# Optimization experiments

Measured on AMD Instinct MI355X. Metric: run time of the kernel, lower is better.

## Reference

```python
import jax, jax.numpy as jnp
import numpy as np

EMB = 512
HEADS = 8

def setup_inputs() -> dict:
    key = jax.random.key(0)
    ks = jax.random.split(key, 9)
    s = 1.0 / np.sqrt(EMB)
    x = jax.random.normal(ks[0], (32, 4096, EMB), dtype=jnp.float32)
    Wq = jax.random.normal(ks[1], (EMB, EMB), dtype=jnp.float32) * s
    bq = jax.random.normal(ks[2], (EMB,), dtype=jnp.float32) * s
    Wk = jax.random.normal(ks[3], (EMB, EMB), dtype=jnp.float32) * s
    bk = jax.random.normal(ks[4], (EMB,), dtype=jnp.float32) * s
    Wv = jax.random.normal(ks[5], (EMB, EMB), dtype=jnp.float32) * s
    bv = jax.random.normal(ks[6], (EMB,), dtype=jnp.float32) * s
    Wo = jax.random.normal(ks[7], (EMB, EMB), dtype=jnp.float32) * s
    bo = jax.random.normal(ks[8], (EMB,), dtype=jnp.float32) * s
    return {"x": x, "Wq": Wq, "bq": bq, "Wk": Wk, "bk": bk,
            "Wv": Wv, "bv": bv, "Wo": Wo, "bo": bo}

def reference(x, Wq, bq, Wk, bk, Wv, bv, Wo, bo):
    b, n, e = x.shape
    h = HEADS
    d = e // h
    scale = jnp.asarray(d ** 0.5, x.dtype)
    # torch Linear: y = x @ W.T + b
    q = (x @ Wq.T + bq).reshape(b, n, h, d)
    k = (x @ Wk.T + bk).reshape(b, n, h, d)
    v = (x @ Wv.T + bv).reshape(b, n, h, d)
    # NOTE: contracts over sequence axis n (faithful to original einsum),
    # producing a (b, h, d, d) feature-feature score matrix.
    qk = jnp.einsum('bnhq,bnhk->bhqk', q, k) / scale
    attn = jax.nn.softmax(qk, axis=-1)  # softmax over head_dim axis
    # dropout is identity at inference
    weighted = jnp.einsum('bhqk,bnhk->bnhq', attn, v).reshape(b, n, e)
    return weighted @ Wo.T + bo
```

## Files before the change

### kernel.cpp

```cpp
#include <hip/hip_runtime.h>
#include <hip/hip_bf16.h>
#include <stdint.h>

#define BATCH 32
#define SEQ   4096
#define EMB   512
#define HEADS 8
#define HD    64
#define SCALE 0.125f

typedef __attribute__((ext_vector_type(8))) short bf16x8;
typedef __attribute__((ext_vector_type(4))) float f32x4;

__device__ __forceinline__ unsigned short f2bf(float f) {
    union { float f; unsigned int u; } v; v.f = f;
    unsigned int u = v.u;
    return (unsigned short)((u + 0x7FFFu + ((u >> 16) & 1u)) >> 16);
}
__device__ __forceinline__ float bf2f(unsigned short h) {
    union { unsigned int u; float f; } v; v.u = ((unsigned int)h) << 16;
    return v.f;
}
__device__ __forceinline__ unsigned int cvtpk(float lo, float hi) {
    unsigned int r;
    asm("v_cvt_pk_bf16_f32 %0, %1, %2" : "=v"(r) : "v"(lo), "v"(hi));
    return r;
}
__device__ __forceinline__ float lo_as_f(unsigned int p) {
    union { unsigned int u; float f; } v; v.u = p << 16; return v.f;
}
__device__ __forceinline__ float hi_as_f(unsigned int p) {
    union { unsigned int u; float f; } v; v.u = p & 0xFFFF0000u; return v.f;
}

#define MFMA16(a, b, c) __builtin_amdgcn_mfma_f32_16x16x32_bf16((a), (b), (c), 0, 0, 0)

union F4 { float4 v; float f[4]; };
struct Regs { F4 a0, a1, a2, a3; };

template <int NCHUNK, bool XBF>
__global__ __launch_bounds__(1024) void k1_gram(const float* __restrict__ x,
                                                float* __restrict__ P,
                                                float* __restrict__ svp,
                                                unsigned short* __restrict__ xbf) {
  constexpr int KC  = SEQ / NCHUNK;
  constexpr int NIT = KC / 32;
  constexpr int NWG = BATCH * 4 * NCHUNK;
  constexpr int PER = NWG / 8;
  const int bid = blockIdx.x;
  const int wk  = (bid & 7) * PER + (bid >> 3);
  const int c   = (NCHUNK == 2) ? (wk & 1) : 0;
  const int tt  = (NCHUNK == 2) ? ((wk >> 1) & 3) : (wk & 3);
  const int b   = (NCHUNK == 2) ? (wk >> 3) : (wk >> 2);
  const int mt = (tt >> 1) & 1, nt = tt & 1;
  const int m0 = mt * 256, n0 = nt * 256;
  const bool diag = (mt == nt);
  const float* __restrict__ xb = x + (size_t)b * SEQ * EMB;
  const int kbeg = c * KC;

  __shared__ unsigned short L[2][64 * 148];
  __shared__ float SR[256][8];

  const int tid  = threadIdx.x;
  const int lane = tid & 63;
  const int wave = tid >> 6;
  const int wr = (wave >> 2) * 64;
  const int wc = (wave & 3) * 64;
  const int er  = lane & 15;
  const int kb8 = (lane >> 4) * 8;

  const int fg   = lane;
  const int kgrp = wave >> 1;
  const bool isB = (wave & 1);
  const int pcol = isB ? n0 : m0;
  const bool active = (!diag) || (!isB);

  f32x4 acc[4][4];
#pragma unroll
  for (int i = 0; i < 4; ++i)
#pragma unroll
    for (int j = 0; j < 4; ++j) acc[i][j] = (f32x4){0.f, 0.f, 0.f, 0.f};

  float sacc[4] = {0.f, 0.f, 0.f, 0.f};

  Regs r0;

  auto loadreg = [&](int t) {
    const float* p = &xb[(size_t)(kbeg + t * 32 + kgrp * 4) * EMB + pcol + fg * 4];
    r0.a0.v = *(const float4*)p;
    r0.a1.v = *(const float4*)(p + EMB);
    r0.a2.v = *(const float4*)(p + 2 * EMB);
    r0.a3.v = *(const float4*)(p + 3 * EMB);
  };

  auto stage = [&](int t) {
    unsigned short* __restrict__ Ld = &L[isB ? 1 : 0][0];
#pragma unroll
    for (int i = 0; i < 4; ++i) {
      uint2 w;
      w.x = cvtpk(r0.a0.f[i], r0.a1.f[i]);
      w.y = cvtpk(r0.a2.f[i], r0.a3.f[i]);
      *(uint2*)&Ld[fg * 148 + i * 36 + kgrp * 4] = w;
    }
    if (diag) {
#pragma unroll
      for (int i = 0; i < 4; ++i)
        sacc[i] += (r0.a0.f[i] + r0.a1.f[i]) + (r0.a2.f[i] + r0.a3.f[i]);
      if (XBF) {
        unsigned short* xp = &xbf[((size_t)b * SEQ + kbeg + t * 32 + kgrp * 4) * EMB + m0 + fg * 4];
        uint2 xr;
        xr.x = cvtpk(r0.a0.f[0], r0.a0.f[1]); xr.y = cvtpk(r0.a0.f[2], r0.a0.f[3]);
        *(uint2*)&xp[0] = xr;
        xr.x = cvtpk(r0.a1.f[0], r0.a1.f[1]); xr.y = cvtpk(r0.a1.f[2], r0.a1.f[3]);
        *(uint2*)&xp[EMB] = xr;
        xr.x = cvtpk(r0.a2.f[0], r0.a2.f[1]); xr.y = cvtpk(r0.a2.f[2], r0.a2.f[3]);
        *(uint2*)&xp[2 * EMB] = xr;
        xr.x = cvtpk(r0.a3.f[0], r0.a3.f[1]); xr.y = cvtpk(r0.a3.f[2], r0.a3.f[3]);
        *(uint2*)&xp[3 * EMB] = xr;
      }
    }
  };

  auto frag = [&](const unsigned short* __restrict__ Ls, int e) -> bf16x8 {
    const int off = (e >> 2) * 148 + (e & 3) * 36 + kb8;
    union { bf16x8 v; uint2 u[2]; } r;
    r.u[0] = *(const uint2*)&Ls[off];
    r.u[1] = *(const uint2*)&Ls[off + 4];
    return r.v;
  };

  if (active) loadreg(0);

  for (int it = 0; it < NIT; ++it) {
    __syncthreads();
    if (active) stage(it);
    __syncthreads();
    if (active && (it + 1 < NIT)) loadreg(it + 1);

    const unsigned short* __restrict__ LAs = &L[0][0];
    const unsigned short* __restrict__ LBs = diag ? LAs : &L[1][0];
    bf16x8 bfr[4];
#pragma unroll
    for (int ns = 0; ns < 4; ++ns) bfr[ns] = frag(LBs, wc + ns * 16 + er);
    {
      bf16x8 a0f = frag(LAs, wr + er);
      bf16x8 a1f = frag(LAs, wr + 16 + er);
#pragma unroll
      for (int ns = 0; ns < 4; ++ns) {
        acc[0][ns] = MFMA16(a0f, bfr[ns], acc[0][ns]);
        acc[1][ns] = MFMA16(a1f, bfr[ns], acc[1][ns]);
      }
    }
    {
      bf16x8 a2f = frag(LAs, wr + 32 + er);
      bf16x8 a3f = frag(LAs, wr + 48 + er);
#pragma unroll
      for (int ns = 0; ns < 4; ++ns) {
        acc[2][ns] = MFMA16(a2f, bfr[ns], acc[2][ns]);
        acc[3][ns] = MFMA16(a3f, bfr[ns], acc[3][ns]);
      }
    }
  }

  float* __restrict__ Pc = P + (size_t)(c * BATCH + b) * EMB * EMB;
#pragma unroll
  for (int ms = 0; ms < 4; ++ms)
#pragma unroll
    for (int ns = 0; ns < 4; ++ns)
#pragma unroll
      for (int r = 0; r < 4; ++r) {
        const int row = m0 + wr + ms * 16 + ((lane >> 4) * 4) + r;
        const int col = n0 + wc + ns * 16 + (lane & 15);
        Pc[(size_t)row * EMB + col] = acc[ms][ns][r];
      }

  if (diag) {
    __syncthreads();
    if (!isB) {
#pragma unroll
      for (int i = 0; i < 4; ++i) SR[fg * 4 + i][kgrp] = sacc[i];
    }
    __syncthreads();
    if (tid < 256) {
      float v = 0.f;
#pragma unroll
      for (int j = 0; j < 8; ++j) v += SR[tid][j];
      svp[(size_t)(c * BATCH + b) * EMB + m0 + tid] = v;
    }
  }
}

template <bool TWO>
__global__ __launch_bounds__(256) void k2a_wqg(const float* __restrict__ Wq,
                                               const float* __restrict__ P,
                                               float* __restrict__ A) {
  const int bid = blockIdx.x;
  const int wk  = (bid & 7) * 64 + (bid >> 3);
  const int b  = wk >> 4;
  const int mt = (wk >> 2) & 3;
  const int nt = wk & 3;
  const int m0 = mt * 128, n0 = nt * 128;
  const float* __restrict__ P0b = P + (size_t)b * EMB * EMB;
  const float* __restrict__ P1b = P + (size_t)(BATCH + b) * EMB * EMB;

  __shared__ unsigned short LA[128][40];
  __shared__ unsigned short LBhi[128][40];
  __shared__ unsigned short LBlo[128][40];

  const int tid  = threadIdx.x;
  const int lane = tid & 63;
  const int wave = tid >> 6;
  const int wr = (wave >> 1) * 64;
  const int wc = (wave & 1) * 64;

  f32x4 acc[4][4];
#pragma unroll
  for (int i = 0; i < 4; ++i)
#pragma unroll
    for (int j = 0; j < 4; ++j) acc[i][j] = (f32x4){0.f, 0.f, 0.f, 0.f};

  const int rA = tid >> 3, fgA = tid & 7;

  F4 ra[4], rb0[4], rb1[4];

  auto loadreg = [&](int k0) {
#pragma unroll
    for (int it = 0; it < 4; ++it) {
      const int r = rA + it * 32;
      ra[it].v  = *(const float4*)&Wq[(size_t)(m0 + r) * EMB + k0 + fgA * 4];
      rb0[it].v = *(const float4*)&P0b[(size_t)(n0 + r) * EMB + k0 + fgA * 4];
      if (TWO)
        rb1[it].v = *(const float4*)&P1b[(size_t)(n0 + r) * EMB + k0 + fgA * 4];
    }
  };

  auto stage = [&]() {
#pragma unroll
    for (int it = 0; it < 4; ++it) {
      const int r = rA + it * 32;
      uint2 u; u.x = cvtpk(ra[it].f[0], ra[it].f[1]); u.y = cvtpk(ra[it].f[2], ra[it].f[3]);
      *(uint2*)&LA[r][fgA * 4] = u;
      float v0 = rb0[it].f[0], v1 = rb0[it].f[1], v2 = rb0[it].f[2], v3 = rb0[it].f[3];
      if (TWO) { v0 += rb1[it].f[0]; v1 += rb1[it].f[1]; v2 += rb1[it].f[2]; v3 += rb1[it].f[3]; }
      uint2 h; h.x = cvtpk(v0, v1); h.y = cvtpk(v2, v3);
      uint2 l;
      l.x = cvtpk(v0 - lo_as_f(h.x), v1 - hi_as_f(h.x));
      l.y = cvtpk(v2 - lo_as_f(h.y), v3 - hi_as_f(h.y));
      *(uint2*)&LBhi[r][fgA * 4] = h;
      *(uint2*)&LBlo[r][fgA * 4] = l;
    }
  };

  loadreg(0);

  for (int k0 = 0; k0 < EMB; k0 += 32) {
    __syncthreads();
    stage();
    __syncthreads();
    if (k0 + 32 < EMB) loadreg(k0 + 32);

    bf16x8 af[4], bh[4], bl[4];
#pragma unroll
    for (int ms = 0; ms < 4; ++ms)
      af[ms] = *(const bf16x8*)&LA[wr + ms*16 + (lane & 15)][(lane >> 4) * 8];
#pragma unroll
    for (int ns = 0; ns < 4; ++ns) {
      bh[ns] = *(const bf16x8*)&LBhi[wc + ns*16 + (lane & 15)][(lane >> 4) * 8];
      bl[ns] = *(const bf16x8*)&LBlo[wc + ns*16 + (lane & 15)][(lane >> 4) * 8];
    }
#pragma unroll
    for (int ms = 0; ms < 4; ++ms)
#pragma unroll
      for (int ns = 0; ns < 4; ++ns) {
        acc[ms][ns] = MFMA16(af[ms], bh[ns], acc[ms][ns]);
        acc[ms][ns] = MFMA16(af[ms], bl[ns], acc[ms][ns]);
      }
  }

  float* __restrict__ Ab = A + (size_t)b * EMB * EMB;
#pragma unroll
  for (int ms = 0; ms < 4; ++ms)
#pragma unroll
    for (int ns = 0; ns < 4; ++ns)
#pragma unroll
      for (int r = 0; r < 4; ++r) {
        const int row = m0 + wr + ms*16 + ((lane >> 4) * 4) + r;
        const int col = n0 + wc + ns*16 + (lane & 15);
        Ab[(size_t)row * EMB + col] = acc[ms][ns][r];
      }
}

template <int NCHUNK>
__global__ __launch_bounds__(256) void k2b_logits(const float* __restrict__ A,
                                                  const float* __restrict__ Wq,
                                                  const float* __restrict__ Wk,
                                                  const float* __restrict__ bq,
                                                  const float* __restrict__ bk,
                                                  const float* __restrict__ svp,
                                                  unsigned short* __restrict__ attn) {
  const int blk = blockIdx.x;
  const int b = blk >> 3;
  const int h = blk & 7;
  const float* __restrict__ Ab = A + (size_t)b * EMB * EMB + (size_t)h * HD * EMB;

  __shared__ unsigned short LAhi[64][40];
  __shared__ unsigned short LAlo[64][40];
  __shared__ unsigned short LB[64][40];
  __shared__ float U[HD], W[HD];

  const int tid  = threadIdx.x;
  const int lane = tid & 63;
  const int wave = tid >> 6;

  const int r8 = tid >> 3, fg8 = tid & 7;

  F4 va[2], vw[2];

  auto loadreg = [&](int k0) {
#pragma unroll
    for (int it = 0; it < 2; ++it) {
      const int r = r8 + it * 32;
      va[it].v = *(const float4*)&Ab[(size_t)r * EMB + k0 + fg8 * 4];
      vw[it].v = *(const float4*)&Wk[(size_t)(h*HD + r) * EMB + k0 + fg8 * 4];
    }
  };

  auto stage = [&]() {
#pragma unroll
    for (int it = 0; it < 2; ++it) {
      const int r = r8 + it * 32;
      uint2 h2; h2.x = cvtpk(va[it].f[0], va[it].f[1]); h2.y = cvtpk(va[it].f[2], va[it].f[3]);
      uint2 l2;
      l2.x = cvtpk(va[it].f[0] - lo_as_f(h2.x), va[it].f[1] - hi_as_f(h2.x));
      l2.y = cvtpk(va[it].f[2] - lo_as_f(h2.y), va[it].f[3] - hi_as_f(h2.y));
      *(uint2*)&LAhi[r][fg8*4] = h2;
      *(uint2*)&LAlo[r][fg8*4] = l2;
      uint2 ub; ub.x = cvtpk(vw[it].f[0], vw[it].f[1]); ub.y = cvtpk(vw[it].f[2], vw[it].f[3]);
      *(uint2*)&LB[r][fg8*4] = ub;
    }
  };

  loadreg(0);

  if (tid < 128) {
    const int q = tid & 63;
    const float* __restrict__ wrow = (tid < 64 ? Wq : Wk) + (size_t)(h * HD + q) * EMB;
    float a = 0.f;
    for (int i = 0; i < EMB; i += 4) {
      const float4 wv = *(const float4*)&wrow[i];
      float4 sv = *(const float4*)&svp[(size_t)b * EMB + i];
      if (NCHUNK == 2) {
        const float4 s1 = *(const float4*)&svp[(size_t)(BATCH + b) * EMB + i];
        sv.x += s1.x; sv.y += s1.y; sv.z += s1.z; sv.w += s1.w;
      }
      a += wv.x*sv.x + wv.y*sv.y + wv.z*sv.z + wv.w*sv.w;
    }
    if (tid < 64) U[q] = a; else W[q] = a;
  }

  f32x4 acc[4];
#pragma unroll
  for (int i = 0; i < 4; ++i) acc[i] = (f32x4){0.f, 0.f, 0.f, 0.f};

  for (int k0 = 0; k0 < EMB; k0 += 32) {
    __syncthreads();
    stage();
    __syncthreads();
    if (k0 + 32 < EMB) loadreg(k0 + 32);

    const bf16x8 ah = *(const bf16x8*)&LAhi[wave*16 + (lane & 15)][(lane >> 4) * 8];
    const bf16x8 al = *(const bf16x8*)&LAlo[wave*16 + (lane & 15)][(lane >> 4) * 8];
#pragma unroll
    for (int ns = 0; ns < 4; ++ns) {
      const bf16x8 bb = *(const bf16x8*)&LB[ns*16 + (lane & 15)][(lane >> 4) * 8];
      acc[ns] = MFMA16(ah, bb, acc[ns]);
      acc[ns] = MFMA16(al, bb, acc[ns]);
    }
  }

  const int colb = lane & 15;
  float bkv[4], wv_[4];
#pragma unroll
  for (int ns = 0; ns < 4; ++ns) {
    bkv[ns] = bk[h*HD + ns*16 + colb];
    wv_[ns] = W[ns*16 + colb];
  }
  unsigned short* __restrict__ ab = attn + (size_t)(b * HEADS + h) * HD * HD;
#pragma unroll
  for (int r = 0; r < 4; ++r) {
    const int row = wave*16 + ((lane >> 4) * 4) + r;
    const float bqv = bq[h*HD + row];
    const float uv  = U[row];
    float vals[4];
#pragma unroll
    for (int ns = 0; ns < 4; ++ns)
      vals[ns] = (acc[ns][r] + uv * bkv[ns] + bqv * wv_[ns] + 4096.f * bqv * bkv[ns]) * SCALE;
    float mx = fmaxf(fmaxf(vals[0], vals[1]), fmaxf(vals[2], vals[3]));
#pragma unroll
    for (int m = 1; m < 16; m <<= 1) mx = fmaxf(mx, __shfl_xor(mx, m));
    float sum = 0.f;
#pragma unroll
    for (int ns = 0; ns < 4; ++ns) { vals[ns] = expf(vals[ns] - mx); sum += vals[ns]; }
#pragma unroll
    for (int m = 1; m < 16; m <<= 1) sum += __shfl_xor(sum, m);
    const float inv = 1.f / sum;
#pragma unroll
    for (int ns = 0; ns < 4; ++ns)
      ab[(size_t)row * HD + ns*16 + colb] = f2bf(vals[ns] * inv);
  }
}

__global__ __launch_bounds__(256) void k3a_c(const float* __restrict__ Wo,
                                             const unsigned short* __restrict__ attn,
                                             unsigned short* __restrict__ C) {
  const int blk = blockIdx.x;
  const int b  = blk >> 5;
  const int h  = (blk >> 2) & 7;
  const int mt = blk & 3;
  const int m0 = mt * 128;

  __shared__ unsigned short LA[128][72];
  __shared__ unsigned short LB[64][72];

  const int tid  = threadIdx.x;
  const int lane = tid & 63;
  const int wave = tid >> 6;

  {
    const int r  = tid >> 4;
    const int fg = tid & 15;
#pragma unroll
    for (int it = 0; it < 8; ++it) {
      const int rr = r + it * 16;
      const float4 v = *(const float4*)&Wo[(size_t)(m0 + rr) * EMB + h*HD + fg * 4];
      uint2 u; u.x = cvtpk(v.x, v.y); u.y = cvtpk(v.z, v.w);
      *(uint2*)&LA[rr][fg * 4] = u;
    }
  }
  {
    const unsigned short* __restrict__ ab = attn + (size_t)(b * HEADS + h) * HD * HD;
#pragma unroll
    for (int it = 0; it < 16; ++it) {
      const int f  = tid + 256 * it;
      const int q  = f >> 6;
      const int kp = f & 63;
      LB[kp][q] = ab[q * HD + kp];
    }
  }
  __syncthreads();

  f32x4 acc[2][4];
#pragma unroll
  for (int i = 0; i < 2; ++i)
#pragma unroll
    for (int j = 0; j < 4; ++j) acc[i][j] = (f32x4){0.f, 0.f, 0.f, 0.f};

#pragma unroll
  for (int kk = 0; kk < 2; ++kk) {
    bf16x8 af[2], bfr[4];
#pragma unroll
    for (int ms = 0; ms < 2; ++ms)
      af[ms] = *(const bf16x8*)&LA[wave*32 + ms*16 + (lane & 15)][kk*32 + (lane >> 4) * 8];
#pragma unroll
    for (int ns = 0; ns < 4; ++ns)
      bfr[ns] = *(const bf16x8*)&LB[ns*16 + (lane & 15)][kk*32 + (lane >> 4) * 8];
#pragma unroll
    for (int ms = 0; ms < 2; ++ms)
#pragma unroll
      for (int ns = 0; ns < 4; ++ns)
        acc[ms][ns] = MFMA16(af[ms], bfr[ns], acc[ms][ns]);
  }

  unsigned short* __restrict__ Cb = C + (size_t)b * EMB * EMB;
#pragma unroll
  for (int ms = 0; ms < 2; ++ms)
#pragma unroll
    for (int ns = 0; ns < 4; ++ns)
#pragma unroll
      for (int r = 0; r < 4; ++r) {
        const int row = m0 + wave*32 + ms*16 + ((lane >> 4) * 4) + r;
        const int col = h*HD + ns*16 + (lane & 15);
        Cb[(size_t)row * EMB + col] = f2bf(acc[ms][ns][r]);
      }
}

__global__ __launch_bounds__(256) void k3b_d(const unsigned short* __restrict__ C,
                                             const float* __restrict__ Wv,
                                             const float* __restrict__ bv,
                                             const float* __restrict__ bo,
                                             unsigned short* __restrict__ D,
                                             float* __restrict__ evec) {
  const int bid = blockIdx.x;
  const int wk  = (bid & 7) * 64 + (bid >> 3);
  const int b  = wk >> 4;
  const int mt = (wk >> 2) & 3;
  const int nt = wk & 3;
  const int m0 = mt * 128, n0 = nt * 128;
  const unsigned short* __restrict__ Cb = C + (size_t)b * EMB * EMB;

  __shared__ unsigned short LA[128][40];
  __shared__ unsigned short LB[32 * 148];
  __shared__ float BV[EMB];

  const int tid  = threadIdx.x;
  const int lane = tid & 63;
  const int wave = tid >> 6;
  const int wr = (wave >> 1) * 64;
  const int wc = (wave & 1) * 64;
  const int er  = lane & 15;
  const int kb8 = (lane >> 4) * 8;

  const bool doE = (nt == 0);
  if (doE) {
    BV[tid] = bv[tid];
    BV[tid + 256] = bv[tid + 256];
  }

  f32x4 acc[4][4];
#pragma unroll
  for (int i = 0; i < 4; ++i)
#pragma unroll
    for (int j = 0; j < 4; ++j) acc[i][j] = (f32x4){0.f, 0.f, 0.f, 0.f};

  float eacc[4] = {0.f, 0.f, 0.f, 0.f};

  const int rA = tid >> 3, fgA = tid & 7;
  const int fgB = tid & 31;
  const int kgB = tid >> 5;

  ushort4 rc[4];
  F4 rb0, rb1, rb2, rb3;

  auto loadreg = [&](int k0) {
#pragma unroll
    for (int it = 0; it < 4; ++it) {
      const int r = rA + it * 32;
      rc[it] = *(const ushort4*)&Cb[(size_t)(m0 + r) * EMB + k0 + fgA * 4];
    }
    const float* p = &Wv[(size_t)(k0 + kgB * 4) * EMB + n0 + fgB * 4];
    rb0.v = *(const float4*)p;
    rb1.v = *(const float4*)(p + EMB);
    rb2.v = *(const float4*)(p + 2 * EMB);
    rb3.v = *(const float4*)(p + 3 * EMB);
  };

  auto stage = [&](int k0) {
    float bvr[4];
    if (doE) {
#pragma unroll
      for (int j = 0; j < 4; ++j) bvr[j] = BV[k0 + fgA * 4 + j];
    }
#pragma unroll
    for (int it = 0; it < 4; ++it) {
      const int r = rA + it * 32;
      *(ushort4*)&LA[r][fgA*4] = rc[it];
      if (doE)
        eacc[it] += bf2f(rc[it].x)*bvr[0] + bf2f(rc[it].y)*bvr[1]
                  + bf2f(rc[it].z)*bvr[2] + bf2f(rc[it].w)*bvr[3];
    }
#pragma unroll
    for (int i = 0; i < 4; ++i) {
      uint2 w;
      w.x = cvtpk(rb0.f[i], rb1.f[i]);
      w.y = cvtpk(rb2.f[i], rb3.f[i]);
      *(uint2*)&LB[fgB * 148 + i * 36 + kgB * 4] = w;
    }
  };

  loadreg(0);

  for (int k0 = 0; k0 < EMB; k0 += 32) {
    __syncthreads();
    stage(k0);
    __syncthreads();
    if (k0 + 32 < EMB) loadreg(k0 + 32);

    bf16x8 af[4], bfr[4];
#pragma unroll
    for (int ms = 0; ms < 4; ++ms)
      af[ms] = *(const bf16x8*)&LA[wr + ms*16 + er][kb8];
#pragma unroll
    for (int ns = 0; ns < 4; ++ns) {
      const int e = wc + ns * 16 + er;
      const int off = (e >> 2) * 148 + (e & 3) * 36 + kb8;
      union { bf16x8 v; uint2 u[2]; } r;
      r.u[0] = *(const uint2*)&LB[off];
      r.u[1] = *(const uint2*)&LB[off + 4];
      bfr[ns] = r.v;
    }
#pragma unroll
    for (int ms = 0; ms < 4; ++ms)
#pragma unroll
      for (int ns = 0; ns < 4; ++ns)
        acc[ms][ns] = MFMA16(af[ms], bfr[ns], acc[ms][ns]);
  }

  unsigned short* __restrict__ Db = D + (size_t)b * EMB * EMB;
#pragma unroll
  for (int ms = 0; ms < 4; ++ms)
#pragma unroll
    for (int ns = 0; ns < 4; ++ns)
#pragma unroll
      for (int r = 0; r < 4; ++r) {
        const int row = m0 + wr + ms*16 + ((lane >> 4) * 4) + r;
        const int col = n0 + wc + ns*16 + (lane & 15);
        Db[(size_t)row * EMB + col] = f2bf(acc[ms][ns][r]);
      }

  if (doE) {
#pragma unroll
    for (int it = 0; it < 4; ++it) {
#pragma unroll
      for (int m = 1; m < 8; m <<= 1) eacc[it] += __shfl_xor(eacc[it], m);
      if (fgA == 0) {
        const int row = m0 + rA + it * 32;
        evec[b * EMB + row] = eacc[it] + bo[row];
      }
    }
  }
}

template <bool XBF>
__global__ __launch_bounds__(1024) void k4_out(const float* __restrict__ x,
                                               const unsigned short* __restrict__ xbf,
                                               const unsigned short* __restrict__ D,
                                               const float* __restrict__ evec,
                                               float* __restrict__ out) {
  const int bid = blockIdx.x;
  const int wk  = (bid & 7) * 128 + (bid >> 3);
  const int b  = wk >> 5;
  const int mt = wk & 31;
  const int m0 = mt * 128;
  const float* __restrict__ xb = x + (size_t)b * SEQ * EMB;
  const unsigned short* __restrict__ xbb = xbf + (size_t)b * SEQ * EMB;
  const unsigned short* __restrict__ Db = D + (size_t)b * EMB * EMB;

  __shared__ unsigned short LA[128 * 40];
  __shared__ unsigned short LB[512 * 40];

  const int tid  = threadIdx.x;
  const int lane = tid & 63;
  const int wave = tid >> 6;
  const int wr = (wave >> 3) * 64;
  const int wc = (wave & 7) * 64;
  const int er  = lane & 15;
  const int kb8 = (lane >> 4) * 8;

  const int rsA = tid >> 3;
  const int kgA = tid & 7;
  const int rsB = tid >> 1;
  const int kgB = (tid & 1) * 16;

  f32x4 acc[4][4];
#pragma unroll
  for (int i = 0; i < 4; ++i)
#pragma unroll
    for (int j = 0; j < 4; ++j) acc[i][j] = (f32x4){0.f, 0.f, 0.f, 0.f};

  uint2 ua;
  F4 fa;
  uint4 ub0, ub1;

  auto loadreg = [&](int k0) {
    if (XBF) {
      ua = *(const uint2*)&xbb[(size_t)(m0 + rsA) * EMB + k0 + kgA * 4];
    } else {
      fa.v = *(const float4*)&xb[(size_t)(m0 + rsA) * EMB + k0 + kgA * 4];
    }
    ub0 = *(const uint4*)&Db[(size_t)rsB * EMB + k0 + kgB];
    ub1 = *(const uint4*)&Db[(size_t)rsB * EMB + k0 + kgB + 8];
  };

  auto stage = [&]() {
    if (XBF) {
      *(uint2*)&LA[rsA * 40 + kgA * 4] = ua;
    } else {
      uint2 w; w.x = cvtpk(fa.f[0], fa.f[1]); w.y = cvtpk(fa.f[2], fa.f[3]);
      *(uint2*)&LA[rsA * 40 + kgA * 4] = w;
    }
    *(uint4*)&LB[rsB * 40 + kgB] = ub0;
    *(uint4*)&LB[rsB * 40 + kgB + 8] = ub1;
  };

  loadreg(0);

  for (int it = 0; it < 16; ++it) {
    __syncthreads();
    stage();
    __syncthreads();
    if (it + 1 < 16) loadreg((it + 1) * 32);

    bf16x8 bfr[4];
#pragma unroll
    for (int ns = 0; ns < 4; ++ns)
      bfr[ns] = *(const bf16x8*)&LB[(wc + ns * 16 + er) * 40 + kb8];
    {
      bf16x8 a0f = *(const bf16x8*)&LA[(wr + er) * 40 + kb8];
      bf16x8 a1f = *(const bf16x8*)&LA[(wr + 16 + er) * 40 + kb8];
#pragma unroll
      for (int ns = 0; ns < 4; ++ns) {
        acc[0][ns] = MFMA16(a0f, bfr[ns], acc[0][ns]);
        acc[1][ns] = MFMA16(a1f, bfr[ns], acc[1][ns]);
      }
    }
    {
      bf16x8 a2f = *(const bf16x8*)&LA[(wr + 32 + er) * 40 + kb8];
      bf16x8 a3f = *(const bf16x8*)&LA[(wr + 48 + er) * 40 + kb8];
#pragma unroll
      for (int ns = 0; ns < 4; ++ns) {
        acc[2][ns] = MFMA16(a2f, bfr[ns], acc[2][ns]);
        acc[3][ns] = MFMA16(a3f, bfr[ns], acc[3][ns]);
      }
    }
  }

  float ev4[4];
#pragma unroll
  for (int ns = 0; ns < 4; ++ns)
    ev4[ns] = evec[b * EMB + wc + ns * 16 + (lane & 15)];

#pragma unroll
  for (int ms = 0; ms < 4; ++ms)
#pragma unroll
    for (int ns = 0; ns < 4; ++ns)
#pragma unroll
      for (int r = 0; r < 4; ++r) {
        const int row = m0 + wr + ms * 16 + ((lane >> 4) * 4) + r;
        const int col = wc + ns * 16 + (lane & 15);
        out[((size_t)b * SEQ + row) * EMB + col] = acc[ms][ns][r] + ev4[ns];
      }
}

extern "C" void kernel_launch(void* const* d_in, const int* in_sizes, int n_in,
                              void* d_out, int out_size, void* d_ws, size_t ws_size,
                              hipStream_t stream) {
  (void)in_sizes; (void)n_in; (void)out_size;
  const float* x  = (const float*)d_in[0];
  const float* Wq = (const float*)d_in[1];
  const float* bq = (const float*)d_in[2];
  const float* Wk = (const float*)d_in[3];
  const float* bk = (const float*)d_in[4];
  const float* Wv = (const float*)d_in[5];
  const float* bv = (const float*)d_in[6];
  const float* Wo = (const float*)d_in[7];
  const float* bo = (const float*)d_in[8];
  float* out = (float*)d_out;

  char* ws = (char*)d_ws;
  const size_t MB = (size_t)1 << 20;
  const size_t XBF_BYTES = (size_t)BATCH * SEQ * EMB * 2;
  const size_t NEED2 = XBF_BYTES + 98 * MB + 256 * 1024;
  const size_t NEED1 = XBF_BYTES + 66 * MB + 256 * 1024;

  if (ws_size >= NEED2) {
    unsigned short* xbf  = (unsigned short*)(ws);
    float*          P    = (float*)(ws + XBF_BYTES);
    unsigned short* Cm   = (unsigned short*)(ws + XBF_BYTES);
    unsigned short* Dm   = (unsigned short*)(ws + XBF_BYTES + 16 * MB);
    float*          A    = (float*)(ws + XBF_BYTES + 64 * MB);
    unsigned short* attn = (unsigned short*)(ws + XBF_BYTES + 96 * MB);
    float*          svp  = (float*)(ws + XBF_BYTES + 98 * MB);
    float*          ev   = (float*)(ws + XBF_BYTES + 98 * MB + 192 * 1024);

    hipLaunchKernelGGL((k1_gram<2, true>), dim3(BATCH * 8),  dim3(1024), 0, stream, x, P, svp, xbf);
    hipLaunchKernelGGL((k2a_wqg<true>),    dim3(BATCH * 16), dim3(256), 0, stream, Wq, P, A);
    hipLaunchKernelGGL((k2b_logits<2>),    dim3(BATCH * 8),  dim3(256), 0, stream, A, Wq, Wk, bq, bk, svp, attn);
    hipLaunchKernelGGL(k3a_c,              dim3(BATCH * 32), dim3(256), 0, stream, Wo, attn, Cm);
    hipLaunchKernelGGL(k3b_d,              dim3(BATCH * 16), dim3(256), 0, stream, Cm, Wv, bv, bo, Dm, ev);
    hipLaunchKernelGGL((k4_out<true>),     dim3(BATCH * 32), dim3(1024), 0, stream, x, xbf, Dm, ev, out);
  } else if (ws_size >= NEED1) {
    unsigned short* xbf  = (unsigned short*)(ws);
    float*          P    = (float*)(ws + XBF_BYTES);
    unsigned short* Cm   = (unsigned short*)(ws + XBF_BYTES);
    unsigned short* Dm   = (unsigned short*)(ws + XBF_BYTES + 16 * MB);
    float*          A    = (float*)(ws + XBF_BYTES + 32 * MB);
    unsigned short* attn = (unsigned short*)(ws + XBF_BYTES + 64 * MB);
    float*          svp  = (float*)(ws + XBF_BYTES + 66 * MB);
    float*          ev   = (float*)(ws + XBF_BYTES + 66 * MB + 192 * 1024);

    hipLaunchKernelGGL((k1_gram<1, true>), dim3(BATCH * 4),  dim3(1024), 0, stream, x, P, svp, xbf);
    hipLaunchKernelGGL((k2a_wqg<false>),   dim3(BATCH * 16), dim3(256), 0, stream, Wq, P, A);
    hipLaunchKernelGGL((k2b_logits<1>),    dim3(BATCH * 8),  dim3(256), 0, stream, A, Wq, Wk, bq, bk, svp, attn);
    hipLaunchKernelGGL(k3a_c,              dim3(BATCH * 32), dim3(256), 0, stream, Wo, attn, Cm);
    hipLaunchKernelGGL(k3b_d,              dim3(BATCH * 16), dim3(256), 0, stream, Cm, Wv, bv, bo, Dm, ev);
    hipLaunchKernelGGL((k4_out<true>),     dim3(BATCH * 32), dim3(1024), 0, stream, x, xbf, Dm, ev, out);
  } else {
    unsigned short* xbf  = (unsigned short*)(ws);
    float*          P    = (float*)(ws);
    unsigned short* Cm   = (unsigned short*)(ws);
    unsigned short* Dm   = (unsigned short*)(ws + 16 * MB);
    float*          A    = (float*)(ws + 32 * MB);
    unsigned short* attn = (unsigned short*)(ws + 64 * MB);
    float*          svp  = (float*)(ws + 66 * MB);
    float*          ev   = (float*)(ws + 66 * MB + 192 * 1024);

    hipLaunchKernelGGL((k1_gram<1, false>), dim3(BATCH * 4),  dim3(1024), 0, stream, x, P, svp, xbf);
    hipLaunchKernelGGL((k2a_wqg<false>),    dim3(BATCH * 16), dim3(256), 0, stream, Wq, P, A);
    hipLaunchKernelGGL((k2b_logits<1>),     dim3(BATCH * 8),  dim3(256), 0, stream, A, Wq, Wk, bq, bk, svp, attn);
    hipLaunchKernelGGL(k3a_c,               dim3(BATCH * 32), dim3(256), 0, stream, Wo, attn, Cm);
    hipLaunchKernelGGL(k3b_d,               dim3(BATCH * 16), dim3(256), 0, stream, Cm, Wv, bv, bo, Dm, ev);
    hipLaunchKernelGGL((k4_out<false>),     dim3(BATCH * 32), dim3(1024), 0, stream, x, xbf, Dm, ev, out);
  }
}
```

Before: 347.7 us.

## Fuse logits-softmax kernel with Wo·attn product and use nontemporal output stores

Merges the attention-logit/softmax kernel with the following C = Wo_h·attn^T kernel into one 512-thread block per (batch, head). Four waves compute the logits while the other four compute the bias vectors and stage Wo into shared memory. The softmax result then stays in shared memory instead of going through global memory. This removes one launch and the attn round trip, but the fused part now runs on only 256 blocks instead of 1024 for the old Wo product, and it uses more LDS per block. The final output stores are also made nontemporal to avoid cache pollution.

New measurement: 363.8 us. 4.7% more time.

```diff
diff --git a/kernel.cpp b/kernel.cpp
--- a/kernel.cpp
+++ b/kernel.cpp
@@ -291,13 +291,14 @@
 }
 
 template <int NCHUNK>
-__global__ __launch_bounds__(256) void k2b_logits(const float* __restrict__ A,
-                                                  const float* __restrict__ Wq,
-                                                  const float* __restrict__ Wk,
-                                                  const float* __restrict__ bq,
-                                                  const float* __restrict__ bk,
-                                                  const float* __restrict__ svp,
-                                                  unsigned short* __restrict__ attn) {
+__global__ __launch_bounds__(512) void k2b3a(const float* __restrict__ A,
+                                             const float* __restrict__ Wq,
+                                             const float* __restrict__ Wk,
+                                             const float* __restrict__ bq,
+                                             const float* __restrict__ bk,
+                                             const float* __restrict__ Wo,
+                                             const float* __restrict__ svp,
+                                             unsigned short* __restrict__ C) {
   const int blk = blockIdx.x;
   const int b = blk >> 3;
   const int h = blk & 7;
@@ -307,10 +308,13 @@
   __shared__ unsigned short LAlo[64][40];
   __shared__ unsigned short LB[64][40];
   __shared__ float U[HD], W[HD];
+  __shared__ unsigned short LBT[64][72];
+  __shared__ unsigned short LWO[256][72];
 
   const int tid  = threadIdx.x;
   const int lane = tid & 63;
   const int wave = tid >> 6;
+  const bool qkw = (wave < 4);
 
   const int r8 = tid >> 3, fg8 = tid & 7;
 
@@ -340,22 +344,25 @@
     }
   };
 
-  loadreg(0);
-
-  if (tid < 128) {
-    const int q = tid & 63;
-    const float* __restrict__ wrow = (tid < 64 ? Wq : Wk) + (size_t)(h * HD + q) * EMB;
-    float a = 0.f;
-    for (int i = 0; i < EMB; i += 4) {
-      const float4 wv = *(const float4*)&wrow[i];
-      float4 sv = *(const float4*)&svp[(size_t)b * EMB + i];
-      if (NCHUNK == 2) {
-        const float4 s1 = *(const float4*)&svp[(size_t)(BATCH + b) * EMB + i];
-        sv.x += s1.x; sv.y += s1.y; sv.z += s1.z; sv.w += s1.w;
-      }
-      a += wv.x*sv.x + wv.y*sv.y + wv.z*sv.z + wv.w*sv.w;
-    }
-    if (tid < 64) U[q] = a; else W[q] = a;
+  if (qkw) loadreg(0);
+
+  if (!qkw) {
+    const int t2 = tid - 256;
+    if (t2 < 128) {
+      const int q = t2 & 63;
+      const float* __restrict__ wrow = (t2 < 64 ? Wq : Wk) + (size_t)(h * HD + q) * EMB;
+      float a = 0.f;
+      for (int i = 0; i < EMB; i += 4) {
+        const float4 wv = *(const float4*)&wrow[i];
+        float4 sv = *(const float4*)&svp[(size_t)b * EMB + i];
+        if (NCHUNK == 2) {
+          const float4 s1 = *(const float4*)&svp[(size_t)(BATCH + b) * EMB + i];
+          sv.x += s1.x; sv.y += s1.y; sv.z += s1.z; sv.w += s1.w;
+        }
+        a += wv.x*sv.x + wv.y*sv.y + wv.z*sv.z + wv.w*sv.w;
+      }
+      if (t2 < 64) U[q] = a; else W[q] = a;
+    }
   }
 
   f32x4 acc[4];
@@ -364,124 +371,113 @@
 
   for (int k0 = 0; k0 < EMB; k0 += 32) {
     __syncthreads();
-    stage();
-    __syncthreads();
-    if (k0 + 32 < EMB) loadreg(k0 + 32);
-
-    const bf16x8 ah = *(const bf16x8*)&LAhi[wave*16 + (lane & 15)][(lane >> 4) * 8];
-    const bf16x8 al = *(const bf16x8*)&LAlo[wave*16 + (lane & 15)][(lane >> 4) * 8];
+    if (qkw) {
+      stage();
+    } else {
+      const int t2 = tid - 256;
+      const int row = (k0 >> 5) * 16 + (t2 >> 4);
+      const int fg = t2 & 15;
+      const float4 v = *(const float4*)&Wo[(size_t)row * EMB + h*HD + fg * 4];
+      uint2 u; u.x = cvtpk(v.x, v.y); u.y = cvtpk(v.z, v.w);
+      *(uint2*)&LWO[row][fg * 4] = u;
+    }
+    __syncthreads();
+    if (qkw) {
+      if (k0 + 32 < EMB) loadreg(k0 + 32);
+
+      const bf16x8 ah = *(const bf16x8*)&LAhi[wave*16 + (lane & 15)][(lane >> 4) * 8];
+      const bf16x8 al = *(const bf16x8*)&LAlo[wave*16 + (lane & 15)][(lane >> 4) * 8];
+#pragma unroll
+      for (int ns = 0; ns < 4; ++ns) {
+        const bf16x8 bb = *(const bf16x8*)&LB[ns*16 + (lane & 15)][(lane >> 4) * 8];
+        acc[ns] = MFMA16(ah, bb, acc[ns]);
+        acc[ns] = MFMA16(al, bb, acc[ns]);
+      }
+    }
+  }
+
+  if (qkw) {
+    const int colb = lane & 15;
+    float bkv[4], wv_[4];
 #pragma unroll
     for (int ns = 0; ns < 4; ++ns) {
-      const bf16x8 bb = *(const bf16x8*)&LB[ns*16 + (lane & 15)][(lane >> 4) * 8];
-      acc[ns] = MFMA16(ah, bb, acc[ns]);
-      acc[ns] = MFMA16(al, bb, acc[ns]);
-    }
-  }
-
-  const int colb = lane & 15;
-  float bkv[4], wv_[4];
-#pragma unroll
-  for (int ns = 0; ns < 4; ++ns) {
-    bkv[ns] = bk[h*HD + ns*16 + colb];
-    wv_[ns] = W[ns*16 + colb];
-  }
-  unsigned short* __restrict__ ab = attn + (size_t)(b * HEADS + h) * HD * HD;
-#pragma unroll
-  for (int r = 0; r < 4; ++r) {
-    const int row = wave*16 + ((lane >> 4) * 4) + r;
-    const float bqv = bq[h*HD + row];
-    const float uv  = U[row];
-    float vals[4];
-#pragma unroll
-    for (int ns = 0; ns < 4; ++ns)
-      vals[ns] = (acc[ns][r] + uv * bkv[ns] + bqv * wv_[ns] + 4096.f * bqv * bkv[ns]) * SCALE;
-    float mx = fmaxf(fmaxf(vals[0], vals[1]), fmaxf(vals[2], vals[3]));
-#pragma unroll
-    for (int m = 1; m < 16; m <<= 1) mx = fmaxf(mx, __shfl_xor(mx, m));
-    float sum = 0.f;
-#pragma unroll
-    for (int ns = 0; ns < 4; ++ns) { vals[ns] = expf(vals[ns] - mx); sum += vals[ns]; }
-#pragma unroll
-    for (int m = 1; m < 16; m <<= 1) sum += __shfl_xor(sum, m);
-    const float inv = 1.f / sum;
-#pragma unroll
-    for (int ns = 0; ns < 4; ++ns)
-      ab[(size_t)row * HD + ns*16 + colb] = f2bf(vals[ns] * inv);
-  }
-}
-
-__global__ __launch_bounds__(256) void k3a_c(const float* __restrict__ Wo,
-                                             const unsigned short* __restrict__ attn,
-                                             unsigned short* __restrict__ C) {
-  const int blk = blockIdx.x;
-  const int b  = blk >> 5;
-  const int h  = (blk >> 2) & 7;
-  const int mt = blk & 3;
-  const int m0 = mt * 128;
-
-  __shared__ unsigned short LA[128][72];
-  __shared__ unsigned short LB[64][72];
-
-  const int tid  = threadIdx.x;
-  const int lane = tid & 63;
-  const int wave = tid >> 6;
-
-  {
-    const int r  = tid >> 4;
-    const int fg = tid & 15;
-#pragma unroll
-    for (int it = 0; it < 8; ++it) {
-      const int rr = r + it * 16;
-      const float4 v = *(const float4*)&Wo[(size_t)(m0 + rr) * EMB + h*HD + fg * 4];
-      uint2 u; u.x = cvtpk(v.x, v.y); u.y = cvtpk(v.z, v.w);
-      *(uint2*)&LA[rr][fg * 4] = u;
-    }
-  }
-  {
-    const unsigned short* __restrict__ ab = attn + (size_t)(b * HEADS + h) * HD * HD;
-#pragma unroll
-    for (int it = 0; it < 16; ++it) {
-      const int f  = tid + 256 * it;
-      const int q  = f >> 6;
-      const int kp = f & 63;
-      LB[kp][q] = ab[q * HD + kp];
+      bkv[ns] = bk[h*HD + ns*16 + colb];
+      wv_[ns] = W[ns*16 + colb];
+    }
+#pragma unroll
+    for (int r = 0; r < 4; ++r) {
+      const int row = wave*16 + ((lane >> 4) * 4) + r;
+      const float bqv = bq[h*HD + row];
+      const float uv  = U[row];
+      float vals[4];
+#pragma unroll
+      for (int ns = 0; ns < 4; ++ns)
+        vals[ns] = (acc[ns][r] + uv * bkv[ns] + bqv * wv_[ns] + 4096.f * bqv * bkv[ns]) * SCALE;
+      float mx = fmaxf(fmaxf(vals[0], vals[1]), fmaxf(vals[2], vals[3]));
+#pragma unroll
+      for (int m = 1; m < 16; m <<= 1) mx = fmaxf(mx, __shfl_xor(mx, m));
+      float sum = 0.f;
+#pragma unroll
+      for (int ns = 0; ns < 4; ++ns) { vals[ns] = expf(vals[ns] - mx); sum += vals[ns]; }
+#pragma unroll
+      for (int m = 1; m < 16; m <<= 1) sum += __shfl_xor(sum, m);
+      const float inv = 1.f / sum;
+#pragma unroll
+      for (int ns = 0; ns < 4; ++ns)
+        LBT[ns*16 + colb][row] = f2bf(vals[ns] * inv);
     }
   }
   __syncthreads();
 
-  f32x4 acc[2][4];
-#pragma unroll
-  for (int i = 0; i < 2; ++i)
-#pragma unroll
-    for (int j = 0; j < 4; ++j) acc[i][j] = (f32x4){0.f, 0.f, 0.f, 0.f};
-
-#pragma unroll
-  for (int kk = 0; kk < 2; ++kk) {
-    bf16x8 af[2], bfr[4];
+  unsigned short* __restrict__ Cb = C + (size_t)b * EMB * EMB;
+  for (int p = 0; p < 2; ++p) {
+    if (p == 1) {
+      __syncthreads();
+      const int rr = tid >> 4;
+      const int fg = tid & 15;
+#pragma unroll
+      for (int j = 0; j < 8; ++j) {
+        const int row = rr + j * 32;
+        const float4 v = *(const float4*)&Wo[(size_t)(256 + row) * EMB + h*HD + fg * 4];
+        uint2 u; u.x = cvtpk(v.x, v.y); u.y = cvtpk(v.z, v.w);
+        *(uint2*)&LWO[row][fg * 4] = u;
+      }
+      __syncthreads();
+    }
+
+    f32x4 acc2[2][4];
+#pragma unroll
+    for (int i = 0; i < 2; ++i)
+#pragma unroll
+      for (int j = 0; j < 4; ++j) acc2[i][j] = (f32x4){0.f, 0.f, 0.f, 0.f};
+
+#pragma unroll
+    for (int kk = 0; kk < 2; ++kk) {
+      bf16x8 af[2], bfr[4];
+#pragma unroll
+      for (int ms = 0; ms < 2; ++ms)
+        af[ms] = *(const bf16x8*)&LWO[wave*32 + ms*16 + (lane & 15)][kk*32 + (lane >> 4) * 8];
+#pragma unroll
+      for (int ns = 0; ns < 4; ++ns)
+        bfr[ns] = *(const bf16x8*)&LBT[ns*16 + (lane & 15)][kk*32 + (lane >> 4) * 8];
+#pragma unroll
+      for (int ms = 0; ms < 2; ++ms)
+#pragma unroll
+        for (int ns = 0; ns < 4; ++ns)
+          acc2[ms][ns] = MFMA16(af[ms], bfr[ns], acc2[ms][ns]);
+    }
+
 #pragma unroll
     for (int ms = 0; ms < 2; ++ms)
-      af[ms] = *(const bf16x8*)&LA[wave*32 + ms*16 + (lane & 15)][kk*32 + (lane >> 4) * 8];
-#pragma unroll
-    for (int ns = 0; ns < 4; ++ns)
-      bfr[ns] = *(const bf16x8*)&LB[ns*16 + (lane & 15)][kk*32 + (lane >> 4) * 8];
-#pragma unroll
-    for (int ms = 0; ms < 2; ++ms)
 #pragma unroll
       for (int ns = 0; ns < 4; ++ns)
-        acc[ms][ns] = MFMA16(af[ms], bfr[ns], acc[ms][ns]);
-  }
-
-  unsigned short* __restrict__ Cb = C + (size_t)b * EMB * EMB;
-#pragma unroll
-  for (int ms = 0; ms < 2; ++ms)
-#pragma unroll
-    for (int ns = 0; ns < 4; ++ns)
-#pragma unroll
-      for (int r = 0; r < 4; ++r) {
-        const int row = m0 + wave*32 + ms*16 + ((lane >> 4) * 4) + r;
-        const int col = h*HD + ns*16 + (lane & 15);
-        Cb[(size_t)row * EMB + col] = f2bf(acc[ms][ns][r]);
-      }
+#pragma unroll
+        for (int r = 0; r < 4; ++r) {
+          const int row = p*256 + wave*32 + ms*16 + ((lane >> 4) * 4) + r;
+          const int col = h*HD + ns*16 + (lane & 15);
+          Cb[(size_t)row * EMB + col] = f2bf(acc2[ms][ns][r]);
+        }
+  }
 }
 
 __global__ __launch_bounds__(256) void k3b_d(const unsigned short* __restrict__ C,
@@ -727,7 +723,8 @@
       for (int r = 0; r < 4; ++r) {
         const int row = m0 + wr + ms * 16 + ((lane >> 4) * 4) + r;
         const int col = wc + ns * 16 + (lane & 15);
-        out[((size_t)b * SEQ + row) * EMB + col] = acc[ms][ns][r] + ev4[ns];
+        __builtin_nontemporal_store(acc[ms][ns][r] + ev4[ns],
+                                    &out[((size_t)b * SEQ + row) * EMB + col]);
       }
 }
 
@@ -758,14 +755,12 @@
     unsigned short* Cm   = (unsigned short*)(ws + XBF_BYTES);
     unsigned short* Dm   = (unsigned short*)(ws + XBF_BYTES + 16 * MB);
     float*          A    = (float*)(ws + XBF_BYTES + 64 * MB);
-    unsigned short* attn = (unsigned short*)(ws + XBF_BYTES + 96 * MB);
     float*          svp  = (float*)(ws + XBF_BYTES + 98 * MB);
     float*          ev   = (float*)(ws + XBF_BYTES + 98 * MB + 192 * 1024);
 
     hipLaunchKernelGGL((k1_gram<2, true>), dim3(BATCH * 8),  dim3(1024), 0, stream, x, P, svp, xbf);
     hipLaunchKernelGGL((k2a_wqg<true>),    dim3(BATCH * 16), dim3(256), 0, stream, Wq, P, A);
-    hipLaunchKernelGGL((k2b_logits<2>),    dim3(BATCH * 8),  dim3(256), 0, stream, A, Wq, Wk, bq, bk, svp, attn);
-    hipLaunchKernelGGL(k3a_c,              dim3(BATCH * 32), dim3(256), 0, stream, Wo, attn, Cm);
+    hipLaunchKernelGGL((k2b3a<2>),         dim3(BATCH * 8),  dim3(512), 0, stream, A, Wq, Wk, bq, bk, Wo, svp, Cm);
     hipLaunchKernelGGL(k3b_d,              dim3(BATCH * 16), dim3(256), 0, stream, Cm, Wv, bv, bo, Dm, ev);
     hipLaunchKernelGGL((k4_out<true>),     dim3(BATCH * 32), dim3(1024), 0, stream, x, xbf, Dm, ev, out);
   } else if (ws_size >= NEED1) {
@@ -774,14 +769,12 @@
     unsigned short* Cm   = (unsigned short*)(ws + XBF_BYTES);
     unsigned short* Dm   = (unsigned short*)(ws + XBF_BYTES + 16 * MB);
     float*          A    = (float*)(ws + XBF_BYTES + 32 * MB);
-    unsigned short* attn = (unsigned short*)(ws + XBF_BYTES + 64 * MB);
     float*          svp  = (float*)(ws + XBF_BYTES + 66 * MB);
     float*          ev   = (float*)(ws + XBF_BYTES + 66 * MB + 192 * 1024);
 
     hipLaunchKernelGGL((k1_gram<1, true>), dim3(BATCH * 4),  dim3(1024), 0, stream, x, P, svp, xbf);
     hipLaunchKernelGGL((k2a_wqg<false>),   dim3(BATCH * 16), dim3(256), 0, stream, Wq, P, A);
-    hipLaunchKernelGGL((k2b_logits<1>),    dim3(BATCH * 8),  dim3(256), 0, stream, A, Wq, Wk, bq, bk, svp, attn);
-    hipLaunchKernelGGL(k3a_c,              dim3(BATCH * 32), dim3(256), 0, stream, Wo, attn, Cm);
+    hipLaunchKernelGGL((k2b3a<1>),         dim3(BATCH * 8),  dim3(512), 0, stream, A, Wq, Wk, bq, bk, Wo, svp, Cm);
     hipLaunchKernelGGL(k3b_d,              dim3(BATCH * 16), dim3(256), 0, stream, Cm, Wv, bv, bo, Dm, ev);
     hipLaunchKernelGGL((k4_out<true>),     dim3(BATCH * 32), dim3(1024), 0, stream, x, xbf, Dm, ev, out);
   } else {
@@ -790,14 +783,12 @@
     unsigned short* Cm   = (unsigned short*)(ws);
     unsigned short* Dm   = (unsigned short*)(ws + 16 * MB);
     float*          A    = (float*)(ws + 32 * MB);
-    unsigned short* attn = (unsigned short*)(ws + 64 * MB);
     float*          svp  = (float*)(ws + 66 * MB);
     float*          ev   = (float*)(ws + 66 * MB + 192 * 1024);
 
     hipLaunchKernelGGL((k1_gram<1, false>), dim3(BATCH * 4),  dim3(1024), 0, stream, x, P, svp, xbf);
     hipLaunchKernelGGL((k2a_wqg<false>),    dim3(BATCH * 16), dim3(256), 0, stream, Wq, P, A);
-    hipLaunchKernelGGL((k2b_logits<1>),     dim3(BATCH * 8),  dim3(256), 0, stream, A, Wq, Wk, bq, bk, svp, attn);
-    hipLaunchKernelGGL(k3a_c,               dim3(BATCH * 32), dim3(256), 0, stream, Wo, attn, Cm);
+    hipLaunchKernelGGL((k2b3a<1>),          dim3(BATCH * 8),  dim3(512), 0, stream, A, Wq, Wk, bq, bk, Wo, svp, Cm);
     hipLaunchKernelGGL(k3b_d,               dim3(BATCH * 16), dim3(256), 0, stream, Cm, Wv, bv, bo, Dm, ev);
     hipLaunchKernelGGL((k4_out<false>),     dim3(BATCH * 32), dim3(1024), 0, stream, x, xbf, Dm, ev, out);
   }
```
